# Kernel optimization log

Measured on AMD Instinct MI355X. Metric: run time of the kernel, lower is better.

The kernel has to match this reference:

```python
import jax, jax.numpy as jnp
import numpy as np

N_NODES = 100000
N_EDGES = 1600000
D_IN = 128
D_HID = 128
D_OUT = 64
N_LAYERS = 3
BN_EPS = 1e-5


def _mlp_block(h, W1, b1, g, be, W2, b2):
    # PyG MLP([c_in, h, h]): Linear -> BatchNorm -> ReLU -> Linear (plain last)
    h = h @ W1 + b1                      # [N, h]
    mu = jnp.mean(h, axis=0)
    var = jnp.var(h, axis=0)             # biased var, BN training-mode stats
    h = (h - mu) * jax.lax.rsqrt(var + BN_EPS) * g + be
    h = jax.nn.relu(h)
    return h @ W2 + b2


def setup_inputs() -> dict:
    key = jax.random.key(0)
    ks = jax.random.split(key, 16)
    s_in = 1.0 / np.sqrt(D_IN)
    s_h = 1.0 / np.sqrt(D_HID)
    x = jax.random.normal(ks[0], (N_NODES, D_IN), dtype=jnp.float32)
    edge_index = jax.random.randint(ks[1], (2, N_EDGES), 0, N_NODES, dtype=jnp.int64)
    return {
        "x": x,
        "edge_index": edge_index,
        # stacked per-conv MLP params (all layers are 128->128->128)
        "W1": jax.random.normal(ks[2], (N_LAYERS, D_IN, D_HID), jnp.float32) * s_in,
        "b1": jnp.zeros((N_LAYERS, D_HID), jnp.float32),
        "g1": jnp.ones((N_LAYERS, D_HID), jnp.float32),
        "be1": jnp.zeros((N_LAYERS, D_HID), jnp.float32),
        "W2": jax.random.normal(ks[3], (N_LAYERS, D_HID, D_HID), jnp.float32) * s_h,
        "b2": jnp.zeros((N_LAYERS, D_HID), jnp.float32),
        # final MLP([h, h, out])
        "fW1": jax.random.normal(ks[4], (D_HID, D_HID), jnp.float32) * s_h,
        "fb1": jnp.zeros((D_HID,), jnp.float32),
        "fg1": jnp.ones((D_HID,), jnp.float32),
        "fbe1": jnp.zeros((D_HID,), jnp.float32),
        "fW2": jax.random.normal(ks[5], (D_HID, D_OUT), jnp.float32) * s_h,
        "fb2": jnp.zeros((D_OUT,), jnp.float32),
    }


def reference(x, edge_index, W1, b1, g1, be1, W2, b2, fW1, fb1, fg1, fbe1, fW2, fb2):
    src, dst = edge_index[0], edge_index[1]
    for l in range(N_LAYERS):
        # GINConv, eps=0: nn((1+eps)*x + sum_{j->i} x_j)
        aggr = jax.ops.segment_sum(x[src], dst, num_segments=N_NODES)  # [N, d]
        h = x + aggr
        x = jax.nn.relu(_mlp_block(h, W1[l], b1[l], g1[l], be1[l], W2[l], b2[l]))
    # final MLP (dropout=0.5 is identity in eval mode)
    return _mlp_block(x, fW1, fb1, fg1, fbe1, fW2, fb2)
```

## Files before the change

### kernel.cpp

```cpp
#include <hip/hip_runtime.h>

#define NN 100000
#define NE 1600000
#define DD 128
#define CAP 56
#define NGROUP 256

static __device__ __forceinline__ unsigned short f2b(float f) {
  unsigned int x = __float_as_uint(f);
  unsigned int r = x + 0x7fffu + ((x >> 16) & 1u);
  return (unsigned short)(r >> 16);
}
static __device__ __forceinline__ float b2f(unsigned short u) {
  return __uint_as_float(((unsigned int)u) << 16);
}

typedef __attribute__((ext_vector_type(8))) short short8;
typedef __attribute__((ext_vector_type(4))) float f32x4;

union V8 {
  uint4 u4;
  short8 s8;
  unsigned short us[8];
};

__global__ void detect_k(const int* __restrict__ ei, int* __restrict__ flag) {
  int v = ei[2 * threadIdx.x + 1];
  unsigned long long b = __ballot(v != 0);
  if (threadIdx.x == 0) *flag = (b == 0ull) ? 1 : 0;
}

__global__ __launch_bounds__(256) void cast_k(const float* __restrict__ x,
                                              unsigned short* __restrict__ x16) {
  size_t i = ((size_t)blockIdx.x * 256 + threadIdx.x) * 8;
  f32x4 a = *(const f32x4*)(x + i);
  f32x4 b = *(const f32x4*)(x + i + 4);
  V8 v;
#pragma unroll
  for (int j = 0; j < 4; ++j) {
    v.us[j] = f2b(a[j]);
    v.us[4 + j] = f2b(b[j]);
  }
  *(uint4*)(x16 + i) = v.u4;
}

__global__ __launch_bounds__(256) void pack_k(const int* __restrict__ ei,
                                              int2* __restrict__ packed,
                                              int* __restrict__ cnt,
                                              float* __restrict__ stats,
                                              const int* __restrict__ flag) {
  const int mode = *flag;
  const int gid = blockIdx.x * 256 + threadIdx.x;
  int s, d;
  if (mode) {
    s = ((const int2*)ei)[gid].x;
    d = ((const int2*)ei)[(size_t)NE + gid].x;
  } else {
    s = ei[gid];
    d = ei[NE + gid];
  }
  packed[gid] = make_int2(s, d);
  if (gid < NN) cnt[gid] = 0;
  if (gid < 8192) stats[gid] = 0.f;
}

__global__ __launch_bounds__(256) void scatter_k(const int2* __restrict__ packed,
                                                 int* __restrict__ cnt,
                                                 int* __restrict__ csr) {
  const int r = blockIdx.x & 7;
  const int g = blockIdx.x >> 3;
  const int lo = r * (NN / 8), hi = lo + (NN / 8);
  for (int e = g * 256 + threadIdx.x; e < NE; e += NGROUP * 256) {
    int2 sd = packed[e];
    if (sd.y >= lo && sd.y < hi) {
      int c = atomicAdd(&cnt[sd.y], 1);
      if (c < CAP) csr[(size_t)sd.y * CAP + c] = sd.x;
    }
  }
}

__global__ __launch_bounds__(256) void wprep_k(const float* __restrict__ W1,
                                               const float* __restrict__ W2,
                                               const float* __restrict__ fW1,
                                               const float* __restrict__ fW2,
                                               unsigned short* __restrict__ wt) {
  int b = blockIdx.x;
  const float* src;
  int moff, N;
  if (b < 192) {
    int m = b >> 6;
    src = W1 + m * 16384;
    moff = m * 16384;
    N = 128;
    b &= 63;
  } else if (b < 384) {
    int m = (b - 192) >> 6;
    src = W2 + m * 16384;
    moff = (3 + m) * 16384;
    N = 128;
    b = (b - 192) & 63;
  } else if (b < 448) {
    src = fW1;
    moff = 6 * 16384;
    N = 128;
    b -= 384;
  } else {
    src = fW2;
    moff = 7 * 16384;
    N = 64;
    b -= 448;
  }
  int idx = b * 256 + threadIdx.x;
  int n = idx >> 7, k = idx & 127;
  if (n < N) wt[moff + idx] = f2b(src[(size_t)k * N + n]);
}

__global__ __launch_bounds__(256) void gather_k(const int* __restrict__ cnt,
                                                const int* __restrict__ csr,
                                                const unsigned short* __restrict__ x16,
                                                unsigned short* __restrict__ h16) {
  const int node = blockIdx.x * 16 + (threadIdx.x >> 4);
  const int l = threadIdx.x & 15;
  const int beg = node * CAP;
  const int end = beg + cnt[node];
  V8 v;
  v.u4 = *(const uint4*)(x16 + (size_t)node * DD + l * 8);
  float a0[8], a1[8], a2[8], a3[8];
#pragma unroll
  for (int j = 0; j < 8; ++j) {
    a0[j] = b2f(v.us[j]);
    a1[j] = 0.f;
    a2[j] = 0.f;
    a3[j] = 0.f;
  }
  int p = beg;
  for (; p + 4 <= end; p += 4) {
    const int s0 = csr[p], s1 = csr[p + 1], s2 = csr[p + 2], s3 = csr[p + 3];
    V8 w0, w1, w2, w3;
    w0.u4 = *(const uint4*)(x16 + (size_t)s0 * DD + l * 8);
    w1.u4 = *(const uint4*)(x16 + (size_t)s1 * DD + l * 8);
    w2.u4 = *(const uint4*)(x16 + (size_t)s2 * DD + l * 8);
    w3.u4 = *(const uint4*)(x16 + (size_t)s3 * DD + l * 8);
#pragma unroll
    for (int j = 0; j < 8; ++j) {
      a0[j] += b2f(w0.us[j]);
      a1[j] += b2f(w1.us[j]);
      a2[j] += b2f(w2.us[j]);
      a3[j] += b2f(w3.us[j]);
    }
  }
  for (; p < end; ++p) {
    const int s0 = csr[p];
    V8 w0;
    w0.u4 = *(const uint4*)(x16 + (size_t)s0 * DD + l * 8);
#pragma unroll
    for (int j = 0; j < 8; ++j) a0[j] += b2f(w0.us[j]);
  }
  V8 o;
#pragma unroll
  for (int j = 0; j < 8; ++j) o.us[j] = f2b((a0[j] + a1[j]) + (a2[j] + a3[j]));
  *(uint4*)(h16 + (size_t)node * DD + l * 8) = o.u4;
}

template <int AMODE, int NCOLS, int EPI, int STATS>
__global__ __launch_bounds__(512) void gemm_k(const unsigned short* __restrict__ Aptr,
                                              const unsigned short* __restrict__ wT,
                                              const float* __restrict__ bias,
                                              const float* __restrict__ bn_stats,
                                              const float* __restrict__ gamma,
                                              const float* __restrict__ beta,
                                              void* __restrict__ Cptr,
                                              float* __restrict__ stats_out) {
  __shared__ unsigned short bT[NCOLS][136];
  __shared__ float biasS[NCOLS];
  __shared__ float scS[128];
  __shared__ float shS[128];
  __shared__ float sS[NCOLS];
  __shared__ float s2S[NCOLS];
  const int tid = threadIdx.x;
  const int wv = tid >> 6;
  const int lane = tid & 63;
  const int l16 = lane & 15;
  const int quad = lane >> 4;
  const int arow = blockIdx.x * 128 + wv * 16 + l16;
  const bool rv = arow < NN;

  V8 afr[4];
#pragma unroll
  for (int kc = 0; kc < 4; ++kc) {
    if (rv) {
      afr[kc].u4 = *(const uint4*)(Aptr + (size_t)arow * DD + kc * 32 + quad * 8);
    } else {
      afr[kc].u4 = make_uint4(0u, 0u, 0u, 0u);
    }
  }

  for (int i = tid; i < NCOLS * 16; i += 512) {
    int n = i >> 4, k8 = (i & 15) << 3;
    *(uint4*)&bT[n][k8] = *(const uint4*)(wT + n * 128 + k8);
  }
  if (tid < NCOLS) biasS[tid] = bias[tid];
  if (AMODE == 2 && tid < 128) {
    float su = 0.f, sq = 0.f;
#pragma unroll
    for (int j = 0; j < 8; ++j) {
      su += bn_stats[j * 256 + tid];
      sq += bn_stats[j * 256 + 128 + tid];
    }
    const float inv_n = 1.0f / (float)NN;
    float mu = su * inv_n;
    float var = sq * inv_n - mu * mu;
    float sc = gamma[tid] * rsqrtf(var + 1e-5f);
    scS[tid] = sc;
    shS[tid] = beta[tid] - mu * sc;
  }
  if (STATS && tid < NCOLS) {
    sS[tid] = 0.f;
    s2S[tid] = 0.f;
  }
  __syncthreads();

  f32x4 acc[NCOLS / 16];
#pragma unroll
  for (int nt = 0; nt < NCOLS / 16; ++nt) acc[nt] = (f32x4)(0.0f);

#pragma unroll
  for (int kc = 0; kc < 4; ++kc) {
    const int k0 = kc * 32 + quad * 8;
    V8 af = afr[kc];
    if (AMODE == 2) {
#pragma unroll
      for (int j = 0; j < 8; ++j) {
        float f = fmaf(b2f(af.us[j]), scS[k0 + j], shS[k0 + j]);
        af.us[j] = f2b(fmaxf(f, 0.0f));
      }
    }
#pragma unroll
    for (int nt = 0; nt < NCOLS / 16; ++nt) {
      V8 bf;
      bf.u4 = *(const uint4*)&bT[nt * 16 + l16][k0];
      acc[nt] = __builtin_amdgcn_mfma_f32_16x16x32_bf16(af.s8, bf.s8, acc[nt], 0, 0, 0);
    }
  }

  const int r0 = blockIdx.x * 128 + wv * 16 + quad * 4;
#pragma unroll
  for (int nt = 0; nt < NCOLS / 16; ++nt) {
    const int col = nt * 16 + l16;
    const float bv = biasS[col];
    float s = 0.f, s2 = 0.f;
#pragma unroll
    for (int i = 0; i < 4; ++i) {
      const int r = r0 + i;
      if (r < NN) {
        float v = acc[nt][i] + bv;
        if (EPI == 1) v = fmaxf(v, 0.0f);
        if (EPI == 2) {
          ((float*)Cptr)[(size_t)r * NCOLS + col] = v;
        } else {
          unsigned short us = f2b(v);
          ((unsigned short*)Cptr)[(size_t)r * NCOLS + col] = us;
          if (STATS) {
            float vr = b2f(us);
            s += vr;
            s2 += vr * vr;
          }
        }
      }
    }
    if (STATS) {
      s += __shfl_xor(s, 16);
      s += __shfl_xor(s, 32);
      s2 += __shfl_xor(s2, 16);
      s2 += __shfl_xor(s2, 32);
      if (quad == 0) {
        atomicAdd(&sS[col], s);
        atomicAdd(&s2S[col], s2);
      }
    }
  }
  if (STATS) {
    __syncthreads();
    if (tid < NCOLS) {
      const int xs = (blockIdx.x & 7) * 256;
      atomicAdd(&stats_out[xs + tid], sS[tid]);
      atomicAdd(&stats_out[xs + 128 + tid], s2S[tid]);
    }
  }
}

extern "C" void kernel_launch(void* const* d_in, const int* in_sizes, int n_in,
                              void* d_out, int out_size, void* d_ws, size_t ws_size,
                              hipStream_t stream) {
  const float* x = (const float*)d_in[0];
  const int* ei = (const int*)d_in[1];
  const float* W1 = (const float*)d_in[2];
  const float* b1 = (const float*)d_in[3];
  const float* g1 = (const float*)d_in[4];
  const float* be1 = (const float*)d_in[5];
  const float* W2 = (const float*)d_in[6];
  const float* b2 = (const float*)d_in[7];
  const float* fW1 = (const float*)d_in[8];
  const float* fb1 = (const float*)d_in[9];
  const float* fg1 = (const float*)d_in[10];
  const float* fbe1 = (const float*)d_in[11];
  const float* fW2 = (const float*)d_in[12];
  const float* fb2 = (const float*)d_in[13];

  char* ws = (char*)d_ws;
  unsigned short* x16 = (unsigned short*)ws;
  unsigned short* h16 = (unsigned short*)(ws + (size_t)25600000);
  unsigned short* t16 = (unsigned short*)(ws + (size_t)51200000);
  int2* packed = (int2*)t16;
  int* csr = (int*)(ws + (size_t)76800000);
  int* cnt = (int*)(ws + (size_t)99200000);
  float* stats = (float*)(ws + (size_t)99600000);
  int* flag = (int*)(ws + (size_t)99632896);
  unsigned short* wt = (unsigned short*)(ws + (size_t)99634176);

  const int vecBlocks = (NN * DD) / (256 * 8);
  const int gemmBlocks = (NN + 127) / 128;
  const int edgeBlocks = NE / 256;
  const int filtBlocks = NGROUP * 8;
  const int nodeBlocks = NN / 16;

  detect_k<<<1, 64, 0, stream>>>(ei, flag);
  cast_k<<<vecBlocks, 256, 0, stream>>>(x, x16);
  pack_k<<<edgeBlocks, 256, 0, stream>>>(ei, packed, cnt, stats, flag);
  wprep_k<<<480, 256, 0, stream>>>(W1, W2, fW1, fW2, wt);
  scatter_k<<<filtBlocks, 256, 0, stream>>>(packed, cnt, csr);

  for (int l = 0; l < 3; ++l) {
    gather_k<<<nodeBlocks, 256, 0, stream>>>(cnt, csr, x16, h16);
    gemm_k<1, 128, 0, 1><<<gemmBlocks, 512, 0, stream>>>(
        h16, wt + (size_t)l * 16384, b1 + l * 128, nullptr, nullptr, nullptr,
        t16, stats + 2048 * l);
    gemm_k<2, 128, 1, 0><<<gemmBlocks, 512, 0, stream>>>(
        t16, wt + (size_t)(3 + l) * 16384, b2 + l * 128, stats + 2048 * l,
        g1 + l * 128, be1 + l * 128, x16, nullptr);
  }

  gemm_k<1, 128, 0, 1><<<gemmBlocks, 512, 0, stream>>>(
      x16, wt + (size_t)6 * 16384, fb1, nullptr, nullptr, nullptr, t16,
      stats + 6144);
  gemm_k<2, 64, 2, 0><<<gemmBlocks, 512, 0, stream>>>(
      t16, wt + (size_t)7 * 16384, fb2, stats + 6144, fg1, fbe1, (float*)d_out,
      nullptr);
}
```

Before: 557.9 us.

## Fuse MLP GEMM pair per layer into cooperative persistent kernel with grid sync

Merges the two GEMMs of each MLP block (linear+BN stats, then BN+ReLU+linear) into one cooperative persistent kernel. A grid-wide sync separates the BatchNorm statistics reduction from the second GEMM. The cast and edge-pack kernels are also merged into one launch. The aim is to cut kernel launches and let each block load its weights once and reuse them across row tiles. The cost is grid sync overhead and occupancy limited to co-resident blocks, and there is a fallback path when cooperative launch is unavailable.

```diff
diff --git a/kernel.cpp b/kernel.cpp
--- a/kernel.cpp
+++ b/kernel.cpp
@@ -1,4 +1,7 @@
 #include <hip/hip_runtime.h>
+#include <hip/hip_cooperative_groups.h>
+
+namespace cg = cooperative_groups;
 
 #define NN 100000
 #define NE 1600000
@@ -30,9 +33,15 @@
   if (threadIdx.x == 0) *flag = (b == 0ull) ? 1 : 0;
 }
 
-__global__ __launch_bounds__(256) void cast_k(const float* __restrict__ x,
-                                              unsigned short* __restrict__ x16) {
-  size_t i = ((size_t)blockIdx.x * 256 + threadIdx.x) * 8;
+__global__ __launch_bounds__(256) void castpack_k(const float* __restrict__ x,
+                                                  unsigned short* __restrict__ x16,
+                                                  const int* __restrict__ ei,
+                                                  int2* __restrict__ packed,
+                                                  int* __restrict__ cnt,
+                                                  float* __restrict__ stats,
+                                                  const int* __restrict__ flag) {
+  const int gid = blockIdx.x * 256 + threadIdx.x;
+  size_t i = (size_t)gid * 8;
   f32x4 a = *(const f32x4*)(x + i);
   f32x4 b = *(const f32x4*)(x + i + 4);
   V8 v;
@@ -42,15 +51,7 @@
     v.us[4 + j] = f2b(b[j]);
   }
   *(uint4*)(x16 + i) = v.u4;
-}
-
-__global__ __launch_bounds__(256) void pack_k(const int* __restrict__ ei,
-                                              int2* __restrict__ packed,
-                                              int* __restrict__ cnt,
-                                              float* __restrict__ stats,
-                                              const int* __restrict__ flag) {
   const int mode = *flag;
-  const int gid = blockIdx.x * 256 + threadIdx.x;
   int s, d;
   if (mode) {
     s = ((const int2*)ei)[gid].x;
@@ -162,6 +163,172 @@
   *(uint4*)(h16 + (size_t)node * DD + l * 8) = o.u4;
 }
 
+template <int SECONDCOLS, int SECEPI>
+__global__ __launch_bounds__(512) void layer_k(const unsigned short* __restrict__ Aptr,
+                                               const unsigned short* __restrict__ wT1,
+                                               const float* __restrict__ bias1,
+                                               const unsigned short* __restrict__ wT2,
+                                               const float* __restrict__ bias2,
+                                               const float* __restrict__ gamma,
+                                               const float* __restrict__ beta,
+                                               unsigned short* __restrict__ t16,
+                                               void* __restrict__ Cptr,
+                                               float* __restrict__ stats,
+                                               int ntiles) {
+  __shared__ unsigned short bT[128][136];
+  __shared__ float scS[128];
+  __shared__ float shS[128];
+  __shared__ float sS[128];
+  __shared__ float s2S[128];
+  const int tid = threadIdx.x;
+  const int wv = tid >> 6;
+  const int lane = tid & 63;
+  const int l16 = lane & 15;
+  const int quad = lane >> 4;
+
+  for (int i = tid; i < 128 * 16; i += 512) {
+    int n = i >> 4, k8 = (i & 15) << 3;
+    *(uint4*)&bT[n][k8] = *(const uint4*)(wT1 + n * 128 + k8);
+  }
+  if (tid < 128) {
+    sS[tid] = 0.f;
+    s2S[tid] = 0.f;
+  }
+  __syncthreads();
+
+  for (int m = blockIdx.x; m < ntiles; m += gridDim.x) {
+    const int arow = m * 128 + wv * 16 + l16;
+    const bool rv = arow < NN;
+    V8 afr[4];
+#pragma unroll
+    for (int kc = 0; kc < 4; ++kc) {
+      if (rv) {
+        afr[kc].u4 = *(const uint4*)(Aptr + (size_t)arow * DD + kc * 32 + quad * 8);
+      } else {
+        afr[kc].u4 = make_uint4(0u, 0u, 0u, 0u);
+      }
+    }
+    f32x4 acc[8];
+#pragma unroll
+    for (int nt = 0; nt < 8; ++nt) acc[nt] = (f32x4)(0.0f);
+#pragma unroll
+    for (int kc = 0; kc < 4; ++kc) {
+      const int k0 = kc * 32 + quad * 8;
+#pragma unroll
+      for (int nt = 0; nt < 8; ++nt) {
+        V8 bf;
+        bf.u4 = *(const uint4*)&bT[nt * 16 + l16][k0];
+        acc[nt] = __builtin_amdgcn_mfma_f32_16x16x32_bf16(afr[kc].s8, bf.s8, acc[nt], 0, 0, 0);
+      }
+    }
+    const int r0 = m * 128 + wv * 16 + quad * 4;
+#pragma unroll
+    for (int nt = 0; nt < 8; ++nt) {
+      const int col = nt * 16 + l16;
+      const float bv = bias1[col];
+      float s = 0.f, s2 = 0.f;
+#pragma unroll
+      for (int i = 0; i < 4; ++i) {
+        const int r = r0 + i;
+        if (r < NN) {
+          unsigned short us = f2b(acc[nt][i] + bv);
+          t16[(size_t)r * 128 + col] = us;
+          float vr = b2f(us);
+          s += vr;
+          s2 += vr * vr;
+        }
+      }
+      s += __shfl_xor(s, 16);
+      s += __shfl_xor(s, 32);
+      s2 += __shfl_xor(s2, 16);
+      s2 += __shfl_xor(s2, 32);
+      if (quad == 0) {
+        atomicAdd(&sS[col], s);
+        atomicAdd(&s2S[col], s2);
+      }
+    }
+  }
+  __syncthreads();
+  if (tid < 128) {
+    const int xs = (blockIdx.x & 7) * 256;
+    atomicAdd(&stats[xs + tid], sS[tid]);
+    atomicAdd(&stats[xs + 128 + tid], s2S[tid]);
+  }
+
+  cg::this_grid().sync();
+
+  for (int i = tid; i < SECONDCOLS * 16; i += 512) {
+    int n = i >> 4, k8 = (i & 15) << 3;
+    *(uint4*)&bT[n][k8] = *(const uint4*)(wT2 + n * 128 + k8);
+  }
+  if (tid < 128) {
+    float su = 0.f, sq = 0.f;
+#pragma unroll
+    for (int j = 0; j < 8; ++j) {
+      su += stats[j * 256 + tid];
+      sq += stats[j * 256 + 128 + tid];
+    }
+    const float inv_n = 1.0f / (float)NN;
+    float mu = su * inv_n;
+    float var = sq * inv_n - mu * mu;
+    float sc = gamma[tid] * rsqrtf(var + 1e-5f);
+    scS[tid] = sc;
+    shS[tid] = beta[tid] - mu * sc;
+  }
+  __syncthreads();
+
+  for (int m = blockIdx.x; m < ntiles; m += gridDim.x) {
+    const int arow = m * 128 + wv * 16 + l16;
+    const bool rv = arow < NN;
+    V8 afr[4];
+#pragma unroll
+    for (int kc = 0; kc < 4; ++kc) {
+      if (rv) {
+        afr[kc].u4 = *(const uint4*)(t16 + (size_t)arow * 128 + kc * 32 + quad * 8);
+      } else {
+        afr[kc].u4 = make_uint4(0u, 0u, 0u, 0u);
+      }
+    }
+    f32x4 acc[SECONDCOLS / 16];
+#pragma unroll
+    for (int nt = 0; nt < SECONDCOLS / 16; ++nt) acc[nt] = (f32x4)(0.0f);
+#pragma unroll
+    for (int kc = 0; kc < 4; ++kc) {
+      const int k0 = kc * 32 + quad * 8;
+      V8 af = afr[kc];
+#pragma unroll
+      for (int j = 0; j < 8; ++j) {
+        float f = fmaf(b2f(af.us[j]), scS[k0 + j], shS[k0 + j]);
+        af.us[j] = f2b(fmaxf(f, 0.0f));
+      }
+#pragma unroll
+      for (int nt = 0; nt < SECONDCOLS / 16; ++nt) {
+        V8 bf;
+        bf.u4 = *(const uint4*)&bT[nt * 16 + l16][k0];
+        acc[nt] = __builtin_amdgcn_mfma_f32_16x16x32_bf16(af.s8, bf.s8, acc[nt], 0, 0, 0);
+      }
+    }
+    const int r0 = m * 128 + wv * 16 + quad * 4;
+#pragma unroll
+    for (int nt = 0; nt < SECONDCOLS / 16; ++nt) {
+      const int col = nt * 16 + l16;
+      const float bv = bias2[col];
+#pragma unroll
+      for (int i = 0; i < 4; ++i) {
+        const int r = r0 + i;
+        if (r < NN) {
+          float v = acc[nt][i] + bv;
+          if (SECEPI == 1) {
+            ((unsigned short*)Cptr)[(size_t)r * SECONDCOLS + col] = f2b(fmaxf(v, 0.0f));
+          } else {
+            ((float*)Cptr)[(size_t)r * SECONDCOLS + col] = v;
+          }
+        }
+      }
+    }
+  }
+}
+
 template <int AMODE, int NCOLS, int EPI, int STATS>
 __global__ __launch_bounds__(512) void gemm_k(const unsigned short* __restrict__ Aptr,
                                               const unsigned short* __restrict__ wT,
@@ -194,7 +361,6 @@
       afr[kc].u4 = make_uint4(0u, 0u, 0u, 0u);
     }
   }
-
   for (int i = tid; i < NCOLS * 16; i += 512) {
     int n = i >> 4, k8 = (i & 15) << 3;
     *(uint4*)&bT[n][k8] = *(const uint4*)(wT + n * 128 + k8);
@@ -223,7 +389,6 @@
   f32x4 acc[NCOLS / 16];
 #pragma unroll
   for (int nt = 0; nt < NCOLS / 16; ++nt) acc[nt] = (f32x4)(0.0f);
-
 #pragma unroll
   for (int kc = 0; kc < 4; ++kc) {
     const int k0 = kc * 32 + quad * 8;
@@ -242,7 +407,6 @@
       acc[nt] = __builtin_amdgcn_mfma_f32_16x16x32_bf16(af.s8, bf.s8, acc[nt], 0, 0, 0);
     }
   }
-
   const int r0 = blockIdx.x * 128 + wv * 16 + quad * 4;
 #pragma unroll
   for (int nt = 0; nt < NCOLS / 16; ++nt) {
@@ -320,30 +484,73 @@
 
   const int vecBlocks = (NN * DD) / (256 * 8);
   const int gemmBlocks = (NN + 127) / 128;
-  const int edgeBlocks = NE / 256;
   const int filtBlocks = NGROUP * 8;
   const int nodeBlocks = NN / 16;
 
+  int dev = 0, coop = 0;
+  hipGetDevice(&dev);
+  hipDeviceGetAttribute(&coop, hipDeviceAttributeCooperativeLaunch, dev);
+  int occA = 0, occB = 0;
+  hipOccupancyMaxActiveBlocksPerMultiprocessor(&occA, layer_k<128, 1>, 512, 0);
+  hipOccupancyMaxActiveBlocksPerMultiprocessor(&occB, layer_k<64, 2>, 512, 0);
+  int gridA = occA > 0 ? occA * 256 : 0;
+  int gridB = occB > 0 ? occB * 256 : 0;
+  if (gridA > gemmBlocks) gridA = gemmBlocks;
+  if (gridB > gemmBlocks) gridB = gemmBlocks;
+  const bool useCoop = (coop != 0) && (gridA > 0) && (gridB > 0);
+
   detect_k<<<1, 64, 0, stream>>>(ei, flag);
-  cast_k<<<vecBlocks, 256, 0, stream>>>(x, x16);
-  pack_k<<<edgeBlocks, 256, 0, stream>>>(ei, packed, cnt, stats, flag);
+  castpack_k<<<vecBlocks, 256, 0, stream>>>(x, x16, ei, packed, cnt, stats, flag);
   wprep_k<<<480, 256, 0, stream>>>(W1, W2, fW1, fW2, wt);
   scatter_k<<<filtBlocks, 256, 0, stream>>>(packed, cnt, csr);
 
+  int ntiles = gemmBlocks;
   for (int l = 0; l < 3; ++l) {
     gather_k<<<nodeBlocks, 256, 0, stream>>>(cnt, csr, x16, h16);
+    if (useCoop) {
+      const unsigned short* Ap = h16;
+      const unsigned short* w1p = wt + (size_t)l * 16384;
+      const float* b1p = b1 + l * 128;
+      const unsigned short* w2p = wt + (size_t)(3 + l) * 16384;
+      const float* b2p = b2 + l * 128;
+      const float* gp = g1 + l * 128;
+      const float* bep = be1 + l * 128;
+      unsigned short* tp = t16;
+      void* cp = (void*)x16;
+      float* sp = stats + 2048 * l;
+      void* args[] = {&Ap, &w1p, &b1p, &w2p, &b2p, &gp, &bep, &tp, &cp, &sp, &ntiles};
+      hipLaunchCooperativeKernel((void*)layer_k<128, 1>, dim3(gridA), dim3(512),
+                                 args, 0, stream);
+    } else {
+      gemm_k<1, 128, 0, 1><<<gemmBlocks, 512, 0, stream>>>(
+          h16, wt + (size_t)l * 16384, b1 + l * 128, nullptr, nullptr, nullptr,
+          t16, stats + 2048 * l);
+      gemm_k<2, 128, 1, 0><<<gemmBlocks, 512, 0, stream>>>(
+          t16, wt + (size_t)(3 + l) * 16384, b2 + l * 128, stats + 2048 * l,
+          g1 + l * 128, be1 + l * 128, x16, nullptr);
+    }
+  }
+
+  if (useCoop) {
+    const unsigned short* Ap = x16;
+    const unsigned short* w1p = wt + (size_t)6 * 16384;
+    const float* b1p = fb1;
+    const unsigned short* w2p = wt + (size_t)7 * 16384;
+    const float* b2p = fb2;
+    const float* gp = fg1;
+    const float* bep = fbe1;
+    unsigned short* tp = t16;
+    void* cp = d_out;
+    float* sp = stats + 6144;
+    void* args[] = {&Ap, &w1p, &b1p, &w2p, &b2p, &gp, &bep, &tp, &cp, &sp, &ntiles};
+    hipLaunchCooperativeKernel((void*)layer_k<64, 2>, dim3(gridB), dim3(512),
+                               args, 0, stream);
+  } else {
     gemm_k<1, 128, 0, 1><<<gemmBlocks, 512, 0, stream>>>(
-        h16, wt + (size_t)l * 16384, b1 + l * 128, nullptr, nullptr, nullptr,
-        t16, stats + 2048 * l);
-    gemm_k<2, 128, 1, 0><<<gemmBlocks, 512, 0, stream>>>(
-        t16, wt + (size_t)(3 + l) * 16384, b2 + l * 128, stats + 2048 * l,
-        g1 + l * 128, be1 + l * 128, x16, nullptr);
-  }
-
-  gemm_k<1, 128, 0, 1><<<gemmBlocks, 512, 0, stream>>>(
-      x16, wt + (size_t)6 * 16384, fb1, nullptr, nullptr, nullptr, t16,
-      stats + 6144);
-  gemm_k<2, 64, 2, 0><<<gemmBlocks, 512, 0, stream>>>(
-      t16, wt + (size_t)7 * 16384, fb2, stats + 6144, fg1, fbe1, (float*)d_out,
-      nullptr);
-}
+        x16, wt + (size_t)6 * 16384, fb1, nullptr, nullptr, nullptr, t16,
+        stats + 6144);
+    gemm_k<2, 64, 2, 0><<<gemmBlocks, 512, 0, stream>>>(
+        t16, wt + (size_t)7 * 16384, fb2, stats + 6144, fg1, fbe1, (float*)d_out,
+        nullptr);
+  }
+}
```

Measured after the change: 555.3 us. About the same (-0.5%).
